# Optimization experiments

Measured on AMD Instinct MI355X. Metric: run time of the kernel, lower is better.

The kernel has to match this reference:

```python
import jax, jax.numpy as jnp
import numpy as np


def setup_inputs() -> dict:
    key = jax.random.key(0)
    k1, k2 = jax.random.split(key)
    B, N, M, K = 8, 4096, 4096, 64
    input1 = jax.random.normal(k1, (B, N, K), dtype=jnp.float32)
    input2 = jax.random.normal(k2, (B, M, K), dtype=jnp.float32)
    return {"input1": input1, "input2": input2}


def reference(input1, input2):
    # Pairwise L2 distances via the ||x||^2 + ||y||^2 - 2<x,y> identity,
    # avoiding the O(B*N*M*K) broadcast-subtraction intermediate.
    x2 = jnp.sum(input1 * input1, axis=-1)                 # [B, N]
    y2 = jnp.sum(input2 * input2, axis=-1)                 # [B, M]
    xy = jnp.einsum('bnk,bmk->bnm', input1, input2)        # [B, N, M]
    sq = x2[:, :, None] + y2[:, None, :] - 2.0 * xy
    D = jnp.sqrt(jnp.maximum(sq, 0.0))                     # [B, N, M]
    dist0 = jnp.mean(jnp.min(D, axis=1), axis=1)           # min over N, mean over M
    dist1 = jnp.mean(jnp.min(D, axis=2), axis=1)           # min over M, mean over N
    loss = jnp.mean(dist0 + dist1)
    return loss
```

## Files before the change

kernel.cpp:

```cpp
#include <hip/hip_runtime.h>

#define BATCH 8
#define NPTS  4096
#define KD    64
#define MQ    8
#define WALK  4
#define FINF  3.0e38f

typedef float f32x4 __attribute__((ext_vector_type(4)));
typedef float f32x2 __attribute__((ext_vector_type(2)));
typedef short s16x8 __attribute__((ext_vector_type(8)));

__device__ __forceinline__ unsigned int f2bf(float f) {
  unsigned int u = __float_as_uint(f);
  u += 0x7FFFu + ((u >> 16) & 1u);
  return u >> 16;
}

__device__ __forceinline__ void stage16(const void* g, void* l) {
  __builtin_amdgcn_global_load_lds((const __attribute__((address_space(1))) void*)g,
                                   (__attribute__((address_space(3))) void*)l, 16, 0, 0);
}

__global__ __launch_bounds__(256)
void prep_kernel(const float* __restrict__ X, const float* __restrict__ Y,
                 unsigned int* __restrict__ Xbf, unsigned int* __restrict__ Ybf,
                 float* __restrict__ x2, float* __restrict__ y2,
                 unsigned int* __restrict__ counter) {
  int gid = blockIdx.x * 256 + threadIdx.x;
  if (gid == 0) *counter = 0;
  int row = gid >> 5;
  int ki  = gid & 31;
  bool isX = row < BATCH * NPTS;
  int r2 = row & (BATCH * NPTS - 1);
  const float* src = isX ? X : Y;
  f32x2 v = *(const f32x2*)(src + (size_t)r2 * KD + ki * 2);
  float s = v[0] * v[0] + v[1] * v[1];
  #pragma unroll
  for (int m = 16; m >= 1; m >>= 1) s += __shfl_xor(s, m, 64);
  unsigned int packed = (f2bf(v[1]) << 16) | f2bf(v[0]);
  (isX ? Xbf : Ybf)[r2 * 32 + ki] = packed;
  if (ki == 0) (isX ? x2 : y2)[r2] = s;
}

__global__ __launch_bounds__(256, 2)
void chamfer_main(const unsigned short* __restrict__ Xbf,
                  const unsigned short* __restrict__ Ybf,
                  const float* __restrict__ x2g, const float* __restrict__ y2g,
                  float* __restrict__ rowpart,
                  float* __restrict__ colpart) {
  __shared__ __align__(16) unsigned short Xs[128 * 64];
  __shared__ __align__(16) unsigned short Ys[2][128 * 64];
  __shared__ float l_cred[2 * 512];

  const int mq = blockIdx.x, ntile = blockIdx.y, b = blockIdx.z;
  const int n0 = ntile * 128;
  const int mbase = mq * 512;
  const int t = threadIdx.x, w = t >> 6, lane = t & 63, c = lane & 15, q = lane >> 4;
  const int wr = (w >> 1) * 64, wc = (w & 1) * 64, rg = w >> 1;

  const int l8 = lane >> 3;
  const int lane_off = l8 * 128 + (((lane & 7) ^ l8) << 4);

  const char* Xg  = (const char*)(Xbf + (size_t)(b * NPTS + n0) * KD);
  const char* Yg0 = (const char*)(Ybf + (size_t)(b * NPTS + mbase) * KD);

  #pragma unroll
  for (int k = 0; k < 4; ++k) {
    int blockoff = (k * 32 + w * 8) * 128;
    int ldsoff   = (k * 256 + w * 64) * 16;
    stage16(Xg  + blockoff + lane_off, (char*)Xs    + ldsoff);
    stage16(Yg0 + blockoff + lane_off, (char*)Ys[0] + ldsoff);
  }

  const float* x2b = x2g + b * NPTS + n0;
  f32x4 x2r[4];
  #pragma unroll
  for (int i = 0; i < 4; ++i) x2r[i] = *(const f32x4*)(x2b + wr + i * 16 + q * 4);

  __syncthreads();

  const int cx = c & 7;
  s16x8 xf[4][2];
  #pragma unroll
  for (int i = 0; i < 4; ++i)
    #pragma unroll
    for (int ks = 0; ks < 2; ++ks)
      xf[i][ks] = *(const s16x8*)&Xs[(wr + i * 16 + c) * 64 + ((((ks << 2) + q) ^ cx) << 3)];

  float rm[4][4];
  #pragma unroll
  for (int i = 0; i < 4; ++i)
    #pragma unroll
    for (int r = 0; r < 4; ++r) rm[i][r] = FINF;

  const float* y2b = y2g + b * NPTS + mbase;
  const f32x4 zacc = {0.f, 0.f, 0.f, 0.f};

  #pragma unroll
  for (int tt = 0; tt < WALK; ++tt) {
    const unsigned short* cur = Ys[tt & 1];

    float y2c[4];
    #pragma unroll
    for (int j = 0; j < 4; ++j) y2c[j] = y2b[tt * 128 + wc + j * 16 + c];

    if (tt < WALK - 1) {
      const char* Ygt = Yg0 + (size_t)(tt + 1) * 128 * 128;
      unsigned short* nb = Ys[(tt + 1) & 1];
      #pragma unroll
      for (int k = 0; k < 4; ++k)
        stage16(Ygt + (k * 32 + w * 8) * 128 + lane_off,
                (char*)nb + (k * 256 + w * 64) * 16);
    }

    float cmj[4];
    #pragma unroll
    for (int j = 0; j < 4; ++j) {
      const unsigned short* yrow = &cur[(wc + j * 16 + c) * 64];
      s16x8 yf0 = *(const s16x8*)&yrow[(q ^ cx) << 3];
      s16x8 yf1 = *(const s16x8*)&yrow[((4 + q) ^ cx) << 3];
      f32x4 acc[4];
      #pragma unroll
      for (int i = 0; i < 4; ++i) {
        f32x4 a0 = __builtin_amdgcn_mfma_f32_16x16x32_bf16(xf[i][0], yf0, zacc, 0, 0, 0);
        acc[i] = __builtin_amdgcn_mfma_f32_16x16x32_bf16(xf[i][1], yf1, a0, 0, 0, 0);
      }
      float cm = FINF;
      #pragma unroll
      for (int i = 0; i < 4; ++i)
        #pragma unroll
        for (int r = 0; r < 4; ++r) {
          float v = acc[i][r];
          rm[i][r] = fminf(rm[i][r], fmaf(-2.f, v, y2c[j]));
          cm = fminf(cm, fmaf(-2.f, v, x2r[i][r]));
        }
      cm = fminf(cm, __shfl_xor(cm, 16, 64));
      cm = fminf(cm, __shfl_xor(cm, 32, 64));
      cmj[j] = cm;
    }
    float cmq = (q == 0) ? cmj[0] : (q == 1) ? cmj[1] : (q == 2) ? cmj[2] : cmj[3];
    l_cred[rg * 512 + tt * 128 + wc + q * 16 + c] = cmq;

    __syncthreads();
  }

  #pragma unroll
  for (int msk = 1; msk <= 8; msk <<= 1)
    #pragma unroll
    for (int i = 0; i < 4; ++i)
      #pragma unroll
      for (int r = 0; r < 4; ++r)
        rm[i][r] = fminf(rm[i][r], __shfl_xor(rm[i][r], msk, 64));
  float* l_redf = (float*)Xs;
  if (c == 0) {
    #pragma unroll
    for (int i = 0; i < 4; ++i) {
      f32x4 v = {rm[i][0], rm[i][1], rm[i][2], rm[i][3]};
      *(f32x4*)&l_redf[w * 64 + i * 16 + q * 4] = v;
    }
  }
  __syncthreads();

  if (t < 128) {
    int g = t >> 6, lr = t & 63;
    float v = fminf(l_redf[(g * 2) * 64 + lr], l_redf[(g * 2 + 1) * 64 + lr]);
    rowpart[mq * (BATCH * NPTS) + b * NPTS + n0 + t] = v + x2b[t];
  } else {
    float* colrow = colpart + (size_t)(ntile * 8 + b) * NPTS + mbase;
    int ct = t - 128;
    #pragma unroll
    for (int u = 0; u < 4; ++u) {
      int cc = ct + u * 128;
      float v = fminf(l_cred[cc], l_cred[512 + cc]);
      colrow[cc] = v + y2b[cc];
    }
  }
}

__global__ __launch_bounds__(256)
void reduce_kernel(const float* __restrict__ rowpart, const float* __restrict__ colpart,
                   float* __restrict__ partials, unsigned int* __restrict__ counter,
                   float* __restrict__ out) {
  int i = blockIdx.x * 256 + threadIdx.x;
  const int TOT = BATCH * NPTS;
  float rv = FINF;
  #pragma unroll
  for (int s = 0; s < MQ; ++s) rv = fminf(rv, rowpart[s * TOT + i]);
  float s0 = sqrtf(fmaxf(rv, 0.f));
  float cv = FINF;
  #pragma unroll
  for (int nt = 0; nt < 32; ++nt) cv = fminf(cv, colpart[nt * TOT + i]);
  s0 += sqrtf(fmaxf(cv, 0.f));
  #pragma unroll
  for (int m = 32; m >= 1; m >>= 1) s0 += __shfl_xor(s0, m, 64);
  __shared__ float wsum[4];
  if ((threadIdx.x & 63) == 0) wsum[threadIdx.x >> 6] = s0;
  __syncthreads();

  if (threadIdx.x < 64) {
    unsigned int ticket = 0;
    if (threadIdx.x == 0) {
      float bsum = wsum[0] + wsum[1] + wsum[2] + wsum[3];
      atomicExch(&partials[blockIdx.x], bsum);
      __threadfence();
      ticket = atomicAdd(counter, 1);
    }
    ticket = __shfl(ticket, 0, 64);
    if (ticket == 127) {
      float v = atomicAdd(&partials[threadIdx.x], 0.0f) +
                atomicAdd(&partials[threadIdx.x + 64], 0.0f);
      #pragma unroll
      for (int m = 32; m >= 1; m >>= 1) v += __shfl_xor(v, m, 64);
      if (threadIdx.x == 0) out[0] = v * (1.0f / (float)TOT);
    }
  }
}

extern "C" void kernel_launch(void* const* d_in, const int* in_sizes, int n_in,
                              void* d_out, int out_size, void* d_ws, size_t ws_size,
                              hipStream_t stream) {
  const float* X = (const float*)d_in[0];
  const float* Y = (const float*)d_in[1];
  float* out = (float*)d_out;

  char* ws = (char*)d_ws;
  unsigned int* Xbf = (unsigned int*)ws;
  unsigned int* Ybf = (unsigned int*)(ws + (4u << 20));
  float* x2 = (float*)(ws + (8u << 20));
  float* y2 = (float*)(ws + (8u << 20) + (128u << 10));
  float* rowpart = (float*)(ws + (8u << 20) + (256u << 10));
  float* colpart = (float*)(ws + (9u << 20) + (256u << 10));
  float* partials = (float*)(ws + (13u << 20) + (256u << 10));
  unsigned int* counter = (unsigned int*)(partials + 128);

  prep_kernel<<<dim3(2 * BATCH * NPTS * 32 / 256), dim3(256), 0, stream>>>(
      X, Y, Xbf, Ybf, x2, y2, counter);

  chamfer_main<<<dim3(MQ, 32, 8), dim3(256), 0, stream>>>(
      (const unsigned short*)Xbf, (const unsigned short*)Ybf, x2, y2, rowpart, colpart);

  reduce_kernel<<<dim3(BATCH * NPTS / 256), dim3(256), 0, stream>>>(
      rowpart, colpart, partials, counter, out);
}
```

Measured before the change: 106.3 us.

## Load MFMA operands directly from global memory instead of LDS staging

Removes the LDS double-buffered staging of X and Y bf16 tiles via global_load_lds and the per-iteration block barriers. Each wave now loads its MFMA fragments straight from global memory into registers, which cuts LDS use sharply and should raise occupancy. In exchange, Y rows are fetched redundantly by the two row-group waves and by every block, which leans on L1/L2, and there is no explicit prefetch to overlap load latency with compute.

```diff
diff --git a/kernel.cpp b/kernel.cpp
--- a/kernel.cpp
+++ b/kernel.cpp
@@ -15,11 +15,6 @@
   unsigned int u = __float_as_uint(f);
   u += 0x7FFFu + ((u >> 16) & 1u);
   return u >> 16;
-}
-
-__device__ __forceinline__ void stage16(const void* g, void* l) {
-  __builtin_amdgcn_global_load_lds((const __attribute__((address_space(1))) void*)g,
-                                   (__attribute__((address_space(3))) void*)l, 16, 0, 0);
 }
 
 __global__ __launch_bounds__(256)
@@ -49,8 +44,7 @@
                   const float* __restrict__ x2g, const float* __restrict__ y2g,
                   float* __restrict__ rowpart,
                   float* __restrict__ colpart) {
-  __shared__ __align__(16) unsigned short Xs[128 * 64];
-  __shared__ __align__(16) unsigned short Ys[2][128 * 64];
+  __shared__ float l_redf[4 * 64];
   __shared__ float l_cred[2 * 512];
 
   const int mq = blockIdx.x, ntile = blockIdx.y, b = blockIdx.z;
@@ -59,18 +53,15 @@
   const int t = threadIdx.x, w = t >> 6, lane = t & 63, c = lane & 15, q = lane >> 4;
   const int wr = (w >> 1) * 64, wc = (w & 1) * 64, rg = w >> 1;
 
-  const int l8 = lane >> 3;
-  const int lane_off = l8 * 128 + (((lane & 7) ^ l8) << 4);
-
-  const char* Xg  = (const char*)(Xbf + (size_t)(b * NPTS + n0) * KD);
-  const char* Yg0 = (const char*)(Ybf + (size_t)(b * NPTS + mbase) * KD);
-
-  #pragma unroll
-  for (int k = 0; k < 4; ++k) {
-    int blockoff = (k * 32 + w * 8) * 128;
-    int ldsoff   = (k * 256 + w * 64) * 16;
-    stage16(Xg  + blockoff + lane_off, (char*)Xs    + ldsoff);
-    stage16(Yg0 + blockoff + lane_off, (char*)Ys[0] + ldsoff);
+  const unsigned short* Xg = Xbf + (size_t)(b * NPTS + n0) * KD;
+  const unsigned short* Yg = Ybf + (size_t)(b * NPTS + mbase) * KD;
+
+  s16x8 xf[4][2];
+  #pragma unroll
+  for (int i = 0; i < 4; ++i) {
+    const unsigned short* xr = Xg + (wr + i * 16 + c) * KD + q * 8;
+    xf[i][0] = *(const s16x8*)xr;
+    xf[i][1] = *(const s16x8*)(xr + 32);
   }
 
   const float* x2b = x2g + b * NPTS + n0;
@@ -78,16 +69,6 @@
   #pragma unroll
   for (int i = 0; i < 4; ++i) x2r[i] = *(const f32x4*)(x2b + wr + i * 16 + q * 4);
 
-  __syncthreads();
-
-  const int cx = c & 7;
-  s16x8 xf[4][2];
-  #pragma unroll
-  for (int i = 0; i < 4; ++i)
-    #pragma unroll
-    for (int ks = 0; ks < 2; ++ks)
-      xf[i][ks] = *(const s16x8*)&Xs[(wr + i * 16 + c) * 64 + ((((ks << 2) + q) ^ cx) << 3)];
-
   float rm[4][4];
   #pragma unroll
   for (int i = 0; i < 4; ++i)
@@ -99,32 +80,24 @@
 
   #pragma unroll
   for (int tt = 0; tt < WALK; ++tt) {
-    const unsigned short* cur = Ys[tt & 1];
-
+    s16x8 yf[4][2];
     float y2c[4];
     #pragma unroll
-    for (int j = 0; j < 4; ++j) y2c[j] = y2b[tt * 128 + wc + j * 16 + c];
-
-    if (tt < WALK - 1) {
-      const char* Ygt = Yg0 + (size_t)(tt + 1) * 128 * 128;
-      unsigned short* nb = Ys[(tt + 1) & 1];
-      #pragma unroll
-      for (int k = 0; k < 4; ++k)
-        stage16(Ygt + (k * 32 + w * 8) * 128 + lane_off,
-                (char*)nb + (k * 256 + w * 64) * 16);
+    for (int j = 0; j < 4; ++j) {
+      const unsigned short* yr = Yg + (tt * 128 + wc + j * 16 + c) * KD + q * 8;
+      yf[j][0] = *(const s16x8*)yr;
+      yf[j][1] = *(const s16x8*)(yr + 32);
+      y2c[j] = y2b[tt * 128 + wc + j * 16 + c];
     }
 
     float cmj[4];
     #pragma unroll
     for (int j = 0; j < 4; ++j) {
-      const unsigned short* yrow = &cur[(wc + j * 16 + c) * 64];
-      s16x8 yf0 = *(const s16x8*)&yrow[(q ^ cx) << 3];
-      s16x8 yf1 = *(const s16x8*)&yrow[((4 + q) ^ cx) << 3];
       f32x4 acc[4];
       #pragma unroll
       for (int i = 0; i < 4; ++i) {
-        f32x4 a0 = __builtin_amdgcn_mfma_f32_16x16x32_bf16(xf[i][0], yf0, zacc, 0, 0, 0);
-        acc[i] = __builtin_amdgcn_mfma_f32_16x16x32_bf16(xf[i][1], yf1, a0, 0, 0, 0);
+        f32x4 a0 = __builtin_amdgcn_mfma_f32_16x16x32_bf16(xf[i][0], yf[j][0], zacc, 0, 0, 0);
+        acc[i] = __builtin_amdgcn_mfma_f32_16x16x32_bf16(xf[i][1], yf[j][1], a0, 0, 0, 0);
       }
       float cm = FINF;
       #pragma unroll
@@ -141,8 +114,6 @@
     }
     float cmq = (q == 0) ? cmj[0] : (q == 1) ? cmj[1] : (q == 2) ? cmj[2] : cmj[3];
     l_cred[rg * 512 + tt * 128 + wc + q * 16 + c] = cmq;
-
-    __syncthreads();
   }
 
   #pragma unroll
@@ -152,7 +123,6 @@
       #pragma unroll
       for (int r = 0; r < 4; ++r)
         rm[i][r] = fminf(rm[i][r], __shfl_xor(rm[i][r], msk, 64));
-  float* l_redf = (float*)Xs;
   if (c == 0) {
     #pragma unroll
     for (int i = 0; i < 4; ++i) {
```

Result: slower. 149.9 us (+41.1%).
